# Performance work log

Hardware: AMD Instinct MI355X
Metric: run time of the kernel (lower is better)

Reference implementation:

```python
import jax, jax.numpy as jnp
import numpy as np

N, E, F_IN, H, EA = 50000, 400000, 16, 128, 8


def _lin(k, fi, fo):
    return jax.random.normal(k, (fi, fo), jnp.float32) / np.float32(np.sqrt(fi))


def setup_inputs() -> dict:
    key = jax.random.key(0)
    ks = jax.random.split(key, 12)
    return {
        "x": jax.random.normal(ks[0], (N, F_IN), jnp.float32),
        "edge_index": jax.random.randint(ks[1], (2, E), 0, N, dtype=jnp.int64),
        "edge_attr": jax.random.normal(ks[2], (E, EA), jnp.float32),
        "layer_num": 3,
        "W_enc": _lin(ks[3], F_IN, H), "b_enc": jnp.zeros((H,), jnp.float32),
        "W_msg": _lin(ks[4], 2 * H, H), "b_msg": jnp.zeros((H,), jnp.float32),
        "W_upd": _lin(ks[5], 2 * H, H), "b_upd": jnp.zeros((H,), jnp.float32),
        "Wn1": _lin(ks[6], H, 64), "bn1": jnp.zeros((64,), jnp.float32),
        "Wn2": _lin(ks[7], 64, 2), "bn2": jnp.zeros((2,), jnp.float32),
        "We1": _lin(ks[8], 2 * H + EA, 128), "be1": jnp.zeros((128,), jnp.float32),
        "We2": _lin(ks[9], 128, 64), "be2": jnp.zeros((64,), jnp.float32),
        "We3": _lin(ks[10], 64, 6), "be3": jnp.zeros((6,), jnp.float32),
    }


def reference(x, edge_index, edge_attr, layer_num,
              W_enc, b_enc, W_msg, b_msg, W_upd, b_upd,
              Wn1, bn1, Wn2, bn2, We1, be1, We2, be2, We3, be3):
    n = x.shape[0]
    src, dst = edge_index[0], edge_index[1]
    # encoder: single linear (MLP with no hidden layers, no act)
    h = x @ W_enc + b_enc  # [N, H]
    # mean-aggregation degree (computed once; edge structure is static)
    deg = jax.ops.segment_sum(jnp.ones((src.shape[0], 1), h.dtype), dst,
                              num_segments=n)
    deg = jnp.maximum(deg, 1.0)
    # repeated graph-network layer + relu (gnn_act=True, dropout_p=0 -> no-op)
    for _ in range(layer_num):
        m = jnp.concatenate([h[src], h[dst]], axis=-1) @ W_msg + b_msg  # [E, H]
        agg = jax.ops.segment_sum(m, dst, num_segments=n) / deg          # [N, H]
        h = jnp.concatenate([h, agg], axis=-1) @ W_upd + b_upd           # [N, H]
        h = jax.nn.relu(h)
    # node head: Linear(H,64)-ReLU-Linear(64,2)
    node_out = jax.nn.relu(h @ Wn1 + bn1) @ Wn2 + bn2
    # edge head: gather src/dst embeddings, concat edge_attr, 3-layer MLP
    ef = jnp.concatenate([h[src], h[dst], edge_attr], axis=-1)  # [E, 2H+EA]
    edge_out = jax.nn.relu(jax.nn.relu(ef @ We1 + be1) @ We2 + be2) @ We3 + be3
    return (node_out, edge_out)
```

## Files before the change

kernel.cpp:

```cpp
#include <hip/hip_runtime.h>
#include <hip/hip_bf16.h>

#define HD 128

typedef __attribute__((ext_vector_type(8))) short bf16x8;
typedef __attribute__((ext_vector_type(4))) float f32x4;

__device__ __forceinline__ ushort f2bf(float f) {
    uint u = __float_as_uint(f);
    return (ushort)((u + 0x7FFFu + ((u >> 16) & 1u)) >> 16);
}
__device__ __forceinline__ float bf2f(ushort h) {
    return __uint_as_float(((uint)h) << 16);
}

__global__ __launch_bounds__(256) void encoder_kernel(
    const float* __restrict__ x, const float* __restrict__ W,
    const float* __restrict__ b, float* __restrict__ h, int N)
{
    int n = blockIdx.x * 2 + (threadIdx.x >> 7);
    int c = threadIdx.x & 127;
    if (n >= N) return;
    const float* xr = x + (size_t)n * 16;
    float acc = b[c];
#pragma unroll
    for (int k = 0; k < 16; ++k)
        acc = fmaf(xr[k], W[k * HD + c], acc);
    h[(size_t)n * HD + c] = acc;
}

__global__ __launch_bounds__(256) void deg_int_kernel(
    const int* __restrict__ dst, int* __restrict__ deg, int E)
{
    int e = blockIdx.x * 256 + threadIdx.x;
    if (e < E) atomicAdd(&deg[dst[e]], 1);
}

__global__ __launch_bounds__(256) void degscale_kernel(
    const int* __restrict__ deg, float* __restrict__ r,
    float* __restrict__ s, int N)
{
    int n = blockIdx.x * 256 + threadIdx.x;
    if (n < N) {
        float c = (float)deg[n];
        float cp = fmaxf(c, 1.0f);
        r[n] = 1.0f / cp;
        s[n] = c / cp;
    }
}

__global__ __launch_bounds__(256) void scan_kernel(
    const int* __restrict__ deg, int* __restrict__ off, int N)
{
    __shared__ int wsum[4];
    const int tid = threadIdx.x;
    const int lane = tid & 63;
    const int wid = tid >> 6;
    int carry = 0;
    for (int base = 0; base < N; base += 256) {
        int i = base + tid;
        int v = (i < N) ? deg[i] : 0;
        int x = v;
#pragma unroll
        for (int d = 1; d < 64; d <<= 1) {
            int y = __shfl_up(x, d);
            if (lane >= d) x += y;
        }
        if (lane == 63) wsum[wid] = x;
        __syncthreads();
        int add = 0;
#pragma unroll
        for (int w = 0; w < 3; ++w)
            if (w < wid) add += wsum[w];
        if (i < N) off[i] = carry + add + x - v;
        carry += wsum[0] + wsum[1] + wsum[2] + wsum[3];
        __syncthreads();
    }
    if (tid == 0) off[N] = carry;
}

__global__ __launch_bounds__(256) void csr_fill_kernel(
    const int* __restrict__ src, const int* __restrict__ dst,
    const int* __restrict__ off, int* __restrict__ cursor,
    int* __restrict__ csr_src, int* __restrict__ csr_dst,
    int* __restrict__ csr_eid, int E)
{
    int e = blockIdx.x * 256 + threadIdx.x;
    if (e < E) {
        int d = dst[e];
        int p = atomicAdd(&cursor[d], 1);
        int pos = off[d] + p;
        csr_src[pos] = src[e];
        csr_dst[pos] = d;
        csr_eid[pos] = e;
    }
}

__global__ __launch_bounds__(256) void pull_kernel(
    const float* __restrict__ h, const int* __restrict__ off,
    const int* __restrict__ csr, const float* __restrict__ r,
    float* __restrict__ S, int N)
{
    int n = blockIdx.x * 4 + (threadIdx.x >> 6);
    if (n >= N) return;
    int lane = threadIdx.x & 63;
    int beg = off[n], end = off[n + 1];
    float ax = 0.0f, ay = 0.0f;
    for (int i = beg; i < end; ++i) {
        int s = csr[i];
        float2 v = *reinterpret_cast<const float2*>(h + (size_t)s * HD + 2 * lane);
        ax += v.x; ay += v.y;
    }
    float rr = r[n];
    *reinterpret_cast<float2*>(S + (size_t)n * HD + 2 * lane) =
        make_float2(ax * rr, ay * rr);
}

__global__ __launch_bounds__(128) void mm2_kernel(
    const float* __restrict__ Wmsg, const float* __restrict__ Wupd,
    float* __restrict__ M)
{
    int b = blockIdx.x;
    int j = threadIdx.x;
    const float* Ar = Wmsg + (size_t)b * 128;
    const float* B  = Wupd + 128 * 128;
    float acc = 0.0f;
#pragma unroll 8
    for (int k = 0; k < 128; ++k)
        acc = fmaf(Ar[k], B[k * 128 + j], acc);
    M[(size_t)b * 128 + j] = acc;
}

__global__ __launch_bounds__(128) void cvec_kernel(
    const float* __restrict__ bmsg, const float* __restrict__ Wupd,
    float* __restrict__ cvec)
{
    int j = threadIdx.x;
    const float* B = Wupd + 128 * 128;
    float acc = 0.0f;
#pragma unroll 8
    for (int k = 0; k < 128; ++k)
        acc = fmaf(bmsg[k], B[k * 128 + j], acc);
    cvec[j] = acc;
}

__global__ __launch_bounds__(256) void wft_build_kernel(
    const float* __restrict__ Wupd, const float* __restrict__ M12,
    ushort* __restrict__ WThi, ushort* __restrict__ WTlo)
{
    int idx = blockIdx.x * 256 + threadIdx.x;
    if (idx >= 384 * 128) return;
    int k = idx >> 7, c = idx & 127;
    float a = (k < 128) ? Wupd[idx] : M12[(size_t)(k - 128) * 128 + c];
    ushort hi = f2bf(a);
    ushort lo = f2bf(a - bf2f(hi));
    WThi[(size_t)c * 384 + k] = hi;
    WTlo[(size_t)c * 384 + k] = lo;
}

__global__ __launch_bounds__(256) void wt_convert_kernel(
    const float* __restrict__ W, ushort* __restrict__ WThi,
    ushort* __restrict__ WTlo, int K, int C)
{
    int idx = blockIdx.x * 256 + threadIdx.x;
    if (idx >= K * C) return;
    int k = idx / C, c = idx % C;
    float a = W[idx];
    ushort hi = f2bf(a);
    ushort lo = f2bf(a - bf2f(hi));
    WThi[c * K + k] = hi;
    WTlo[c * K + k] = lo;
}

__global__ __launch_bounds__(256) void gemm_fused_kernel(
    const float* __restrict__ h, const float* __restrict__ S,
    const float* __restrict__ ss,
    const ushort* __restrict__ WT_hi, const ushort* __restrict__ WT_lo,
    const float* __restrict__ bupd, const float* __restrict__ cvec,
    float* __restrict__ out, int N)
{
    __shared__ __align__(16) ushort Ahi_s[64][40];
    __shared__ __align__(16) ushort Alo_s[64][40];
    __shared__ __align__(16) ushort Bhi_s[128][40];
    __shared__ __align__(16) ushort Blo_s[128][40];

    const int tid    = threadIdx.x;
    const int n_base = blockIdx.x * 64;
    const int sa_row = tid >> 2;
    const int sa_k4  = (tid & 3) * 4;
    const int sa_ng  = min(n_base + sa_row, N - 1);
    const float scA  = ss[sa_ng];
    const int sb_c = tid & 127;
    const int sb_h = (tid >> 7) * 16;
    const int lane = tid & 63, wv = tid >> 6;
    const int fr = lane & 15;
    const int fk = (lane >> 4) * 8;

    f32x4 acc[8];
#pragma unroll
    for (int t = 0; t < 8; ++t) acc[t] = (f32x4){0.f, 0.f, 0.f, 0.f};

    for (int s = 0; s < 12; ++s) {
        const int k0 = s * 32;
        __syncthreads();
        const int part = k0 >> 7;
        const int kof  = k0 & 127;
        const float* Ab = (part == 1) ? S : h;
        const float  sc = (part == 2) ? scA : 1.0f;
#pragma unroll
        for (int ch = 0; ch < 32; ch += 16) {
            float4 v = *reinterpret_cast<const float4*>(
                Ab + (size_t)sa_ng * HD + kof + ch + sa_k4);
            float vv[4] = {v.x * sc, v.y * sc, v.z * sc, v.w * sc};
            ushort4 hi, lo;
            hi.x = f2bf(vv[0]); lo.x = f2bf(vv[0] - bf2f(hi.x));
            hi.y = f2bf(vv[1]); lo.y = f2bf(vv[1] - bf2f(hi.y));
            hi.z = f2bf(vv[2]); lo.z = f2bf(vv[2] - bf2f(hi.z));
            hi.w = f2bf(vv[3]); lo.w = f2bf(vv[3] - bf2f(hi.w));
            *reinterpret_cast<ushort4*>(&Ahi_s[sa_row][ch + sa_k4]) = hi;
            *reinterpret_cast<ushort4*>(&Alo_s[sa_row][ch + sa_k4]) = lo;
        }
        {
            const ushort* ph = WT_hi + (size_t)sb_c * 384 + k0 + sb_h;
            const ushort* pl = WT_lo + (size_t)sb_c * 384 + k0 + sb_h;
            *reinterpret_cast<uint4*>(&Bhi_s[sb_c][sb_h])     = *reinterpret_cast<const uint4*>(ph);
            *reinterpret_cast<uint4*>(&Bhi_s[sb_c][sb_h + 8]) = *reinterpret_cast<const uint4*>(ph + 8);
            *reinterpret_cast<uint4*>(&Blo_s[sb_c][sb_h])     = *reinterpret_cast<const uint4*>(pl);
            *reinterpret_cast<uint4*>(&Blo_s[sb_c][sb_h + 8]) = *reinterpret_cast<const uint4*>(pl + 8);
        }
        __syncthreads();
        bf16x8 ah = *reinterpret_cast<bf16x8*>(&Ahi_s[wv * 16 + fr][fk]);
        bf16x8 al = *reinterpret_cast<bf16x8*>(&Alo_s[wv * 16 + fr][fk]);
#pragma unroll
        for (int t = 0; t < 8; ++t) {
            bf16x8 bh = *reinterpret_cast<bf16x8*>(&Bhi_s[t * 16 + fr][fk]);
            bf16x8 bl = *reinterpret_cast<bf16x8*>(&Blo_s[t * 16 + fr][fk]);
            acc[t] = __builtin_amdgcn_mfma_f32_16x16x32_bf16(ah, bh, acc[t], 0, 0, 0);
            acc[t] = __builtin_amdgcn_mfma_f32_16x16x32_bf16(al, bh, acc[t], 0, 0, 0);
            acc[t] = __builtin_amdgcn_mfma_f32_16x16x32_bf16(ah, bl, acc[t], 0, 0, 0);
        }
    }
#pragma unroll
    for (int reg = 0; reg < 4; ++reg) {
        int n = n_base + wv * 16 + (lane >> 4) * 4 + reg;
        if (n < N) {
            float sv = ss[n];
#pragma unroll
            for (int t = 0; t < 8; ++t) {
                int c = t * 16 + fr;
                float v = acc[t][reg] + bupd[c] + sv * cvec[c];
                out[(size_t)n * HD + c] = fmaxf(v, 0.0f);
            }
        }
    }
}

__global__ __launch_bounds__(256) void gemm_mfma_kernel(
    const float* __restrict__ A0, const float* __restrict__ A1,
    const float* __restrict__ s1,
    const ushort* __restrict__ WT_hi, const ushort* __restrict__ WT_lo,
    int wstride, int kw0,
    const float* __restrict__ bias, const float* __restrict__ bscale,
    float* __restrict__ out, int N, int K, int relu)
{
    __shared__ __align__(16) ushort Ahi_s[64][40];
    __shared__ __align__(16) ushort Alo_s[64][40];
    __shared__ __align__(16) ushort Bhi_s[128][40];
    __shared__ __align__(16) ushort Blo_s[128][40];

    const int tid    = threadIdx.x;
    const int n_base = blockIdx.x * 64;
    const int sa_row = tid >> 2;
    const int sa_k4  = (tid & 3) * 4;
    const int sa_ng  = min(n_base + sa_row, N - 1);
    const float scA1 = s1 ? s1[sa_ng] : 1.0f;
    const int sb_c = tid & 127;
    const int sb_h = (tid >> 7) * 16;
    const int lane = tid & 63, wv = tid >> 6;
    const int fr = lane & 15;
    const int fk = (lane >> 4) * 8;

    f32x4 acc[8];
#pragma unroll
    for (int t = 0; t < 8; ++t) acc[t] = (f32x4){0.f, 0.f, 0.f, 0.f};

    const int nsteps = K >> 5;
    for (int s = 0; s < nsteps; ++s) {
        const int k0 = s * 32;
        __syncthreads();
        const float* Ab; int kof; float sc;
        if (K == 256 && k0 >= 128) { Ab = A1; kof = k0 - 128; sc = scA1; }
        else                       { Ab = A0; kof = k0;       sc = 1.0f; }
#pragma unroll
        for (int ch = 0; ch < 32; ch += 16) {
            float4 v = *reinterpret_cast<const float4*>(
                Ab + (size_t)sa_ng * HD + kof + ch + sa_k4);
            float vv[4] = {v.x * sc, v.y * sc, v.z * sc, v.w * sc};
            ushort4 hi, lo;
            hi.x = f2bf(vv[0]); lo.x = f2bf(vv[0] - bf2f(hi.x));
            hi.y = f2bf(vv[1]); lo.y = f2bf(vv[1] - bf2f(hi.y));
            hi.z = f2bf(vv[2]); lo.z = f2bf(vv[2] - bf2f(hi.z));
            hi.w = f2bf(vv[3]); lo.w = f2bf(vv[3] - bf2f(hi.w));
            *reinterpret_cast<ushort4*>(&Ahi_s[sa_row][ch + sa_k4]) = hi;
            *reinterpret_cast<ushort4*>(&Alo_s[sa_row][ch + sa_k4]) = lo;
        }
        {
            const ushort* ph = WT_hi + (size_t)sb_c * wstride + kw0 + k0 + sb_h;
            const ushort* pl = WT_lo + (size_t)sb_c * wstride + kw0 + k0 + sb_h;
            *reinterpret_cast<uint4*>(&Bhi_s[sb_c][sb_h])     = *reinterpret_cast<const uint4*>(ph);
            *reinterpret_cast<uint4*>(&Bhi_s[sb_c][sb_h + 8]) = *reinterpret_cast<const uint4*>(ph + 8);
            *reinterpret_cast<uint4*>(&Blo_s[sb_c][sb_h])     = *reinterpret_cast<const uint4*>(pl);
            *reinterpret_cast<uint4*>(&Blo_s[sb_c][sb_h + 8]) = *reinterpret_cast<const uint4*>(pl + 8);
        }
        __syncthreads();
        bf16x8 ah = *reinterpret_cast<bf16x8*>(&Ahi_s[wv * 16 + fr][fk]);
        bf16x8 al = *reinterpret_cast<bf16x8*>(&Alo_s[wv * 16 + fr][fk]);
#pragma unroll
        for (int t = 0; t < 8; ++t) {
            bf16x8 bh = *reinterpret_cast<bf16x8*>(&Bhi_s[t * 16 + fr][fk]);
            bf16x8 bl = *reinterpret_cast<bf16x8*>(&Blo_s[t * 16 + fr][fk]);
            acc[t] = __builtin_amdgcn_mfma_f32_16x16x32_bf16(ah, bh, acc[t], 0, 0, 0);
            acc[t] = __builtin_amdgcn_mfma_f32_16x16x32_bf16(al, bh, acc[t], 0, 0, 0);
            acc[t] = __builtin_amdgcn_mfma_f32_16x16x32_bf16(ah, bl, acc[t], 0, 0, 0);
        }
    }
#pragma unroll
    for (int reg = 0; reg < 4; ++reg) {
        int n = n_base + wv * 16 + (lane >> 4) * 4 + reg;
        if (n < N) {
            float bs = bscale ? bscale[n] : 1.0f;
#pragma unroll
            for (int t = 0; t < 8; ++t) {
                int c = t * 16 + fr;
                float v = acc[t][reg] + (bias ? bias[c] * bs : 0.0f);
                out[(size_t)n * HD + c] = relu ? fmaxf(v, 0.0f) : v;
            }
        }
    }
}

__global__ __launch_bounds__(256) void node_head_kernel(
    const float* __restrict__ h,
    const float* __restrict__ W1, const float* __restrict__ b1,
    const float* __restrict__ W2, const float* __restrict__ b2,
    float* __restrict__ out, int N)
{
    int n = blockIdx.x * 4 + (threadIdx.x >> 6);
    int lane = threadIdx.x & 63;
    if (n >= N) return;
    const float* hr = h + (size_t)n * HD;
    float t = b1[lane];
#pragma unroll 16
    for (int k = 0; k < HD; ++k)
        t = fmaf(hr[k], W1[k * 64 + lane], t);
    t = fmaxf(t, 0.0f);
    float o0 = t * W2[lane * 2 + 0];
    float o1 = t * W2[lane * 2 + 1];
#pragma unroll
    for (int sft = 32; sft > 0; sft >>= 1) {
        o0 += __shfl_xor(o0, sft);
        o1 += __shfl_xor(o1, sft);
    }
    if (lane == 0) {
        out[(size_t)n * 2 + 0] = o0 + b2[0];
        out[(size_t)n * 2 + 1] = o1 + b2[1];
    }
}

__global__ __launch_bounds__(256) void edge_head_kernel(
    const float* __restrict__ P, const float* __restrict__ Q,
    const int* __restrict__ csr_src, const int* __restrict__ csr_dst,
    const int* __restrict__ csr_eid,
    const float* __restrict__ ea,
    const float* __restrict__ W1c, const float* __restrict__ b1,
    const ushort* __restrict__ W2Th, const ushort* __restrict__ W2Tl,
    const float* __restrict__ b2,
    const float* __restrict__ W3, const float* __restrict__ b3,
    float* __restrict__ out, int E)
{
    __shared__ float t1pre[64][132];
    __shared__ float ea_s[64][8];
    __shared__ int sn_s[64], dn_s[64], eid_s[64];

    const int tid  = threadIdx.x;
    const int base = blockIdx.x * 64;
    const int lane = tid & 63, wv = tid >> 6;

    if (tid < 64) {
        int slot = min(base + tid, E - 1);
        sn_s[tid]  = csr_src[slot];
        dn_s[tid]  = csr_dst[slot];
        eid_s[tid] = csr_eid[slot];
    }
    __syncthreads();

    if (tid < 128) {
        int e = tid >> 1, q = (tid & 1) * 4;
        float4 v = *reinterpret_cast<const float4*>(ea + (size_t)eid_s[e] * 8 + q);
        *reinterpret_cast<float4*>(&ea_s[e][q]) = v;
    }

    float2 b1v = *reinterpret_cast<const float2*>(b1 + 2 * lane);
    float2 pv[16], qv[16];
#pragma unroll
    for (int i = 0; i < 16; ++i) {
        int e = wv * 16 + i;
        pv[i] = *reinterpret_cast<const float2*>(P + (size_t)sn_s[e] * HD + 2 * lane);
    }
#pragma unroll
    for (int i = 0; i < 16; ++i) {
        int e = wv * 16 + i;
        qv[i] = *reinterpret_cast<const float2*>(Q + (size_t)dn_s[e] * HD + 2 * lane);
    }
#pragma unroll
    for (int i = 0; i < 16; ++i) {
        int e = wv * 16 + i;
        t1pre[e][2 * lane]     = pv[i].x + qv[i].x + b1v.x;
        t1pre[e][2 * lane + 1] = pv[i].y + qv[i].y + b1v.y;
    }
    __syncthreads();

    const int fr = lane & 15, hi16 = lane >> 4, fk = hi16 * 8;
    const int eL = wv * 16 + fr;
    float eav[8];
#pragma unroll
    for (int k = 0; k < 8; ++k) eav[k] = ea_s[eL][k];

    bf16x8 ah[4], al[4];
#pragma unroll
    for (int kt = 0; kt < 4; ++kt) {
        const int c0 = kt * 32 + fk;
        float4 v0 = *reinterpret_cast<float4*>(&t1pre[eL][c0]);
        float4 v1 = *reinterpret_cast<float4*>(&t1pre[eL][c0 + 4]);
        float v[8] = {v0.x, v0.y, v0.z, v0.w, v1.x, v1.y, v1.z, v1.w};
#pragma unroll
        for (int k = 0; k < 8; ++k) {
            float4 w0 = *reinterpret_cast<const float4*>(W1c + k * HD + c0);
            float4 w1 = *reinterpret_cast<const float4*>(W1c + k * HD + c0 + 4);
            v[0] = fmaf(eav[k], w0.x, v[0]); v[1] = fmaf(eav[k], w0.y, v[1]);
            v[2] = fmaf(eav[k], w0.z, v[2]); v[3] = fmaf(eav[k], w0.w, v[3]);
            v[4] = fmaf(eav[k], w1.x, v[4]); v[5] = fmaf(eav[k], w1.y, v[5]);
            v[6] = fmaf(eav[k], w1.z, v[6]); v[7] = fmaf(eav[k], w1.w, v[7]);
        }
#pragma unroll
        for (int j = 0; j < 8; ++j) {
            float t = fmaxf(v[j], 0.0f);
            ushort h = f2bf(t);
            ushort l = f2bf(t - bf2f(h));
            ah[kt][j] = (short)h;
            al[kt][j] = (short)l;
        }
    }

    f32x4 acc[4];
#pragma unroll
    for (int t = 0; t < 4; ++t) acc[t] = (f32x4){0.f, 0.f, 0.f, 0.f};
#pragma unroll
    for (int kt = 0; kt < 4; ++kt) {
#pragma unroll
        for (int t = 0; t < 4; ++t) {
            const size_t boff = (size_t)(t * 16 + fr) * 128 + kt * 32 + fk;
            bf16x8 bh = *reinterpret_cast<const bf16x8*>(W2Th + boff);
            bf16x8 bl = *reinterpret_cast<const bf16x8*>(W2Tl + boff);
            acc[t] = __builtin_amdgcn_mfma_f32_16x16x32_bf16(ah[kt], bh, acc[t], 0, 0, 0);
            acc[t] = __builtin_amdgcn_mfma_f32_16x16x32_bf16(al[kt], bh, acc[t], 0, 0, 0);
            acc[t] = __builtin_amdgcn_mfma_f32_16x16x32_bf16(ah[kt], bl, acc[t], 0, 0, 0);
        }
    }

    float b2v[4];
#pragma unroll
    for (int t = 0; t < 4; ++t) b2v[t] = b2[t * 16 + fr];
#pragma unroll
    for (int reg = 0; reg < 4; ++reg) {
        int erow = wv * 16 + hi16 * 4 + reg;
        float p[6];
#pragma unroll
        for (int j = 0; j < 6; ++j) p[j] = 0.0f;
#pragma unroll
        for (int t = 0; t < 4; ++t) {
            int c = t * 16 + fr;
            float t2v = fmaxf(acc[t][reg] + b2v[t], 0.0f);
#pragma unroll
            for (int j = 0; j < 6; ++j)
                p[j] = fmaf(t2v, W3[c * 6 + j], p[j]);
        }
#pragma unroll
        for (int j = 0; j < 6; ++j) {
#pragma unroll
            for (int sft = 1; sft < 16; sft <<= 1)
                p[j] += __shfl_xor(p[j], sft);
        }
        int oslot = base + erow;
        if (fr < 6 && oslot < E) {
            out[(size_t)eid_s[erow] * 6 + fr] = p[fr] + b3[fr];
        }
    }
}

extern "C" void kernel_launch(void* const* d_in, const int* in_sizes, int n_in,
                              void* d_out, int out_size, void* d_ws, size_t ws_size,
                              hipStream_t stream)
{
    (void)n_in; (void)out_size; (void)ws_size;
    const float* x     = (const float*)d_in[0];
    const int*   ei    = (const int*)d_in[1];
    const float* eattr = (const float*)d_in[2];
    const float* Wenc = (const float*)d_in[4];
    const float* benc = (const float*)d_in[5];
    const float* Wmsg = (const float*)d_in[6];
    const float* bmsg = (const float*)d_in[7];
    const float* Wupd = (const float*)d_in[8];
    const float* bupd = (const float*)d_in[9];
    const float* Wn1  = (const float*)d_in[10];
    const float* bn1  = (const float*)d_in[11];
    const float* Wn2  = (const float*)d_in[12];
    const float* bn2  = (const float*)d_in[13];
    const float* We1  = (const float*)d_in[14];
    const float* be1  = (const float*)d_in[15];
    const float* We2  = (const float*)d_in[16];
    const float* be2  = (const float*)d_in[17];
    const float* We3  = (const float*)d_in[18];
    const float* be3  = (const float*)d_in[19];

    const int N = in_sizes[0] / 16;
    const int E = in_sizes[1] / 2;
    const int* src = ei;
    const int* dst = ei + E;

    float* h0   = (float*)d_ws;
    float* h1   = h0 + (size_t)N * HD;
    float* S    = h1 + (size_t)N * HD;
    float* Qb   = S  + (size_t)N * HD;
    float* rs   = Qb + (size_t)N * HD;
    float* ss   = rs + N;
    int* deg_i  = (int*)(ss + N);
    int* off    = deg_i + N;
    int* cursor = off + N + 1;
    int* csr_s  = cursor + N;
    int* csr_d  = csr_s + E;
    int* csr_e  = csr_d + E;
    float* fM   = (float*)(((uintptr_t)(csr_e + E) + 255) & ~(uintptr_t)255);
    float* M12  = fM;
    float* cvec = fM + 32768;
    ushort* wt  = (ushort*)(cvec + 128);
    ushort* wft_hi = wt;
    ushort* wft_lo = wft_hi + 49152;
    ushort* wte_hi = wft_lo + 49152;
    ushort* wte_lo = wte_hi + 32768;
    ushort* w2t_hi = wte_lo + 32768;
    ushort* w2t_lo = w2t_hi + 8192;

    float* node_out = (float*)d_out;
    float* edge_out = node_out + (size_t)N * 2;

    hipMemsetAsync(deg_i, 0, (size_t)N * sizeof(int), stream);
    hipMemsetAsync(cursor, 0, (size_t)N * sizeof(int), stream);
    deg_int_kernel<<<(E + 255) / 256, 256, 0, stream>>>(dst, deg_i, E);
    scan_kernel<<<1, 256, 0, stream>>>(deg_i, off, N);
    degscale_kernel<<<(N + 255) / 256, 256, 0, stream>>>(deg_i, rs, ss, N);
    csr_fill_kernel<<<(E + 255) / 256, 256, 0, stream>>>(
        src, dst, off, cursor, csr_s, csr_d, csr_e, E);

    mm2_kernel<<<256, 128, 0, stream>>>(Wmsg, Wupd, M12);
    cvec_kernel<<<1, 128, 0, stream>>>(bmsg, Wupd, cvec);
    wft_build_kernel<<<192, 256, 0, stream>>>(Wupd, M12, wft_hi, wft_lo);
    wt_convert_kernel<<<128, 256, 0, stream>>>(We1, wte_hi, wte_lo, 256, 128);
    wt_convert_kernel<<<32,  256, 0, stream>>>(We2, w2t_hi, w2t_lo, 128, 64);

    encoder_kernel<<<(N + 1) / 2, 256, 0, stream>>>(x, Wenc, benc, h0, N);

    const int gblocks = (N + 63) / 64;
    float* hc = h0;
    float* hn = h1;
    for (int l = 0; l < 3; ++l) {
        pull_kernel<<<(N + 3) / 4, 256, 0, stream>>>(hc, off, csr_s, rs, S, N);
        gemm_fused_kernel<<<gblocks, 256, 0, stream>>>(
            hc, S, ss, wft_hi, wft_lo, bupd, cvec, hn, N);
        float* t = hc; hc = hn; hn = t;
    }

    float* Pb = S;
    gemm_mfma_kernel<<<gblocks, 256, 0, stream>>>(
        hc, nullptr, nullptr, wte_hi, wte_lo, 256, 0, nullptr, nullptr, Pb, N, 128, 0);
    gemm_mfma_kernel<<<gblocks, 256, 0, stream>>>(
        hc, nullptr, nullptr, wte_hi, wte_lo, 256, 128, nullptr, nullptr, Qb, N, 128, 0);

    node_head_kernel<<<(N + 3) / 4, 256, 0, stream>>>(
        hc, Wn1, bn1, Wn2, bn2, node_out, N);
    edge_head_kernel<<<(E + 63) / 64, 256, 0, stream>>>(
        Pb, Qb, csr_s, csr_d, csr_e, eattr, We1 + (size_t)256 * HD, be1,
        w2t_hi, w2t_lo, be2, We3, be3, edge_out, E);
}
```

Before: 942.8 us.

## Unroll pull aggregation and load edge-head features directly into MFMA fragments

Result: faster. 863.2 us (-8.4%).

```diff
diff --git a/kernel.cpp b/kernel.cpp
--- a/kernel.cpp
+++ b/kernel.cpp
@@ -106,7 +106,17 @@
     int lane = threadIdx.x & 63;
     int beg = off[n], end = off[n + 1];
     float ax = 0.0f, ay = 0.0f;
-    for (int i = beg; i < end; ++i) {
+    int i = beg;
+    for (; i + 3 < end; i += 4) {
+        int s0 = csr[i], s1 = csr[i + 1], s2 = csr[i + 2], s3 = csr[i + 3];
+        float2 v0 = *reinterpret_cast<const float2*>(h + (size_t)s0 * HD + 2 * lane);
+        float2 v1 = *reinterpret_cast<const float2*>(h + (size_t)s1 * HD + 2 * lane);
+        float2 v2 = *reinterpret_cast<const float2*>(h + (size_t)s2 * HD + 2 * lane);
+        float2 v3 = *reinterpret_cast<const float2*>(h + (size_t)s3 * HD + 2 * lane);
+        ax += (v0.x + v1.x) + (v2.x + v3.x);
+        ay += (v0.y + v1.y) + (v2.y + v3.y);
+    }
+    for (; i < end; ++i) {
         int s = csr[i];
         float2 v = *reinterpret_cast<const float2*>(h + (size_t)s * HD + 2 * lane);
         ax += v.x; ay += v.y;
@@ -378,61 +388,41 @@
     const float* __restrict__ W3, const float* __restrict__ b3,
     float* __restrict__ out, int E)
 {
-    __shared__ float t1pre[64][132];
-    __shared__ float ea_s[64][8];
-    __shared__ int sn_s[64], dn_s[64], eid_s[64];
-
     const int tid  = threadIdx.x;
     const int base = blockIdx.x * 64;
     const int lane = tid & 63, wv = tid >> 6;
-
-    if (tid < 64) {
-        int slot = min(base + tid, E - 1);
-        sn_s[tid]  = csr_src[slot];
-        dn_s[tid]  = csr_dst[slot];
-        eid_s[tid] = csr_eid[slot];
-    }
-    __syncthreads();
-
-    if (tid < 128) {
-        int e = tid >> 1, q = (tid & 1) * 4;
-        float4 v = *reinterpret_cast<const float4*>(ea + (size_t)eid_s[e] * 8 + q);
-        *reinterpret_cast<float4*>(&ea_s[e][q]) = v;
-    }
-
-    float2 b1v = *reinterpret_cast<const float2*>(b1 + 2 * lane);
-    float2 pv[16], qv[16];
-#pragma unroll
-    for (int i = 0; i < 16; ++i) {
-        int e = wv * 16 + i;
-        pv[i] = *reinterpret_cast<const float2*>(P + (size_t)sn_s[e] * HD + 2 * lane);
-    }
-#pragma unroll
-    for (int i = 0; i < 16; ++i) {
-        int e = wv * 16 + i;
-        qv[i] = *reinterpret_cast<const float2*>(Q + (size_t)dn_s[e] * HD + 2 * lane);
-    }
-#pragma unroll
-    for (int i = 0; i < 16; ++i) {
-        int e = wv * 16 + i;
-        t1pre[e][2 * lane]     = pv[i].x + qv[i].x + b1v.x;
-        t1pre[e][2 * lane + 1] = pv[i].y + qv[i].y + b1v.y;
-    }
-    __syncthreads();
-
-    const int fr = lane & 15, hi16 = lane >> 4, fk = hi16 * 8;
-    const int eL = wv * 16 + fr;
+    const int fr = lane & 15;
+    const int hi16 = lane >> 4;
+    const int fk = hi16 * 8;
+
+    const int slot = min(base + wv * 16 + fr, E - 1);
+    const int sn  = csr_src[slot];
+    const int dn  = csr_dst[slot];
+    const int eid = csr_eid[slot];
+
     float eav[8];
-#pragma unroll
-    for (int k = 0; k < 8; ++k) eav[k] = ea_s[eL][k];
+    {
+        float4 e0 = *reinterpret_cast<const float4*>(ea + (size_t)eid * 8);
+        float4 e1 = *reinterpret_cast<const float4*>(ea + (size_t)eid * 8 + 4);
+        eav[0] = e0.x; eav[1] = e0.y; eav[2] = e0.z; eav[3] = e0.w;
+        eav[4] = e1.x; eav[5] = e1.y; eav[6] = e1.z; eav[7] = e1.w;
+    }
 
     bf16x8 ah[4], al[4];
 #pragma unroll
     for (int kt = 0; kt < 4; ++kt) {
         const int c0 = kt * 32 + fk;
-        float4 v0 = *reinterpret_cast<float4*>(&t1pre[eL][c0]);
-        float4 v1 = *reinterpret_cast<float4*>(&t1pre[eL][c0 + 4]);
-        float v[8] = {v0.x, v0.y, v0.z, v0.w, v1.x, v1.y, v1.z, v1.w};
+        float4 p0 = *reinterpret_cast<const float4*>(P + (size_t)sn * HD + c0);
+        float4 p1 = *reinterpret_cast<const float4*>(P + (size_t)sn * HD + c0 + 4);
+        float4 q0 = *reinterpret_cast<const float4*>(Q + (size_t)dn * HD + c0);
+        float4 q1 = *reinterpret_cast<const float4*>(Q + (size_t)dn * HD + c0 + 4);
+        float4 b0 = *reinterpret_cast<const float4*>(b1 + c0);
+        float4 b1v = *reinterpret_cast<const float4*>(b1 + c0 + 4);
+        float v[8];
+        v[0] = p0.x + q0.x + b0.x;  v[1] = p0.y + q0.y + b0.y;
+        v[2] = p0.z + q0.z + b0.z;  v[3] = p0.w + q0.w + b0.w;
+        v[4] = p1.x + q1.x + b1v.x; v[5] = p1.y + q1.y + b1v.y;
+        v[6] = p1.z + q1.z + b1v.z; v[7] = p1.w + q1.w + b1v.w;
 #pragma unroll
         for (int k = 0; k < 8; ++k) {
             float4 w0 = *reinterpret_cast<const float4*>(W1c + k * HD + c0);
@@ -493,7 +483,8 @@
         }
         int oslot = base + erow;
         if (fr < 6 && oslot < E) {
-            out[(size_t)eid_s[erow] * 6 + fr] = p[fr] + b3[fr];
+            int oeid = csr_eid[oslot];
+            out[(size_t)oeid * 6 + fr] = p[fr] + b3[fr];
         }
     }
 }
```
